# Performance work log

Hardware: AMD Instinct MI355X
Metric: run time of the kernel (lower is better)

The kernel has to match this reference:

```python
import jax, jax.numpy as jnp
import numpy as np

N, I, C, P, K = 16, 4096, 16, 16, 8
NI = N * I
E_RAND = 524288
CP = C + P


def setup_inputs() -> dict:
    key = jax.random.key(0)
    ks = jax.random.split(key, 14)
    x = jax.random.normal(ks[0], (N, I, C), dtype=jnp.float32)
    # random edges (stand-in for data-dependent kmeans complete subgraphs) + self loops
    src = jax.random.randint(ks[1], (E_RAND,), 0, NI)
    dst = jax.random.randint(ks[2], (E_RAND,), 0, NI)
    loops = jnp.arange(NI)
    edge_index = jnp.stack([jnp.concatenate([src, loops]),
                            jnp.concatenate([dst, loops])], axis=0)  # [2, E]
    # cluster labels: point p of cloud n -> cluster (p % K) + n*K, every cluster non-empty
    cluster_index = (jnp.arange(NI) % K) + (jnp.arange(NI) // I) * K
    sC = 1.0 / np.sqrt(C)
    sCP = 1.0 / np.sqrt(CP)
    return {
        "x": x,
        "edge_index": edge_index,
        "cluster_index": cluster_index,
        "F_W": jax.random.normal(ks[3], (C, C * CP), dtype=jnp.float32) * sC,
        "F_b": jnp.zeros((C * CP,), dtype=jnp.float32),
        "W_W": jax.random.normal(ks[4], (C, C * CP), dtype=jnp.float32) * sC,
        "W_b": jnp.zeros((C * CP,), dtype=jnp.float32),
        "M_W": jax.random.normal(ks[5], (CP, 1), dtype=jnp.float32) * sCP,
        "M_b": jnp.zeros((1,), dtype=jnp.float32),
        "B": jax.random.normal(ks[6], (CP,), dtype=jnp.float32),
        "mlp1_W": jax.random.normal(ks[7], (CP, CP), dtype=jnp.float32) * sCP,
        "mlp1_b": jnp.zeros((CP,), dtype=jnp.float32),
        "mlp2_W": jax.random.normal(ks[8], (CP, CP), dtype=jnp.float32) * sCP,
        "mlp2_b": jnp.zeros((CP,), dtype=jnp.float32),
        "sc_W": jax.random.normal(ks[9], (CP, CP), dtype=jnp.float32) * sCP,
        "sc_b": jnp.zeros((CP,), dtype=jnp.float32),
        "lr": jnp.asarray(1.0, dtype=jnp.float32),
    }


def _shrinking_unit(x, edge_index, cluster_index,
                    F_W, F_b, W_W, W_b, M_W, M_b, B,
                    mlp1_W, mlp1_b, mlp2_W, mlp2_b, sc_W, sc_b, lr):
    xf = x.reshape(-1, C)                      # [NI, C]
    src, dst = edge_index[0], edge_index[1]    # message flows src(j) -> dst(i)
    x_i = xf[dst]                              # [E, C]
    x_j = xf[src]
    # message: per-edge transform matrix F(x_j - x_i) in R^{(C+P) x C} applied to x_i
    msg = ((x_j - x_i) @ F_W + F_b).reshape(-1, CP, C)   # [E, CP, C]
    msg = jnp.einsum('epc,ec->ep', msg, x_i)             # [E, CP]
    # mean aggregation over incoming edges (self-loops guarantee deg >= 1)
    deg = jax.ops.segment_sum(jnp.ones_like(dst, dtype=x.dtype), dst, num_segments=NI)
    aggr = jax.ops.segment_sum(msg, dst, num_segments=NI) / deg[:, None]   # [NI, CP]
    # update
    weight = aggr @ M_W + M_b                             # [NI, 1]
    aggr = aggr * weight
    transform = (xf @ W_W + W_b).reshape(-1, CP, C)       # [NI, CP, C]
    aggr = aggr + jnp.einsum('npc,nc->np', transform, xf)
    conv = jax.nn.sigmoid(aggr + B).reshape(N, I, CP)     # [N, I, CP]
    # Aggregation module: pad x to CP, squeeze-excite style softmax gate
    x_pad = jnp.pad(x, ((0, 0), (0, 0), (0, P)))          # [N, I, CP]
    S1 = jnp.mean(x_pad, axis=1)                          # [N, CP]
    S2 = jnp.mean(conv, axis=1)
    Z1 = S1 @ mlp1_W + mlp1_b
    Z2 = S2 @ mlp2_W + mlp2_b
    M = jax.nn.softmax(jnp.stack([Z1, Z2], axis=0), axis=0)  # [2, N, CP]
    fused = M[0][:, None, :] * x_pad + M[1][:, None, :] * conv  # [N, I, CP]
    # MaxPool over clusters
    pooled = jax.ops.segment_max(fused.reshape(-1, CP), cluster_index,
                                 num_segments=K * N).reshape(N, K, CP)
    # SelfCorrelation: residual MLP scaled by learnable lambda
    pf = pooled.reshape(-1, CP)
    out = (pf + lr * (pf @ sc_W + sc_b)).reshape(N, K, CP)
    return out


def reference(x, edge_index, cluster_index, F_W, F_b, W_W, W_b, M_W, M_b, B,
              mlp1_W, mlp1_b, mlp2_W, mlp2_b, sc_W, sc_b, lr):
    return _shrinking_unit(x, edge_index, cluster_index, F_W, F_b, W_W, W_b,
                           M_W, M_b, B, mlp1_W, mlp1_b, mlp2_W, mlp2_b,
                           sc_W, sc_b, lr)
```

## Files before the change

### kernel.cpp

```cpp
#include <hip/hip_runtime.h>
#include <hip/hip_bf16.h>


#define POOL_NBLK 256

__device__ __forceinline__ unsigned fmap(float f) {
    unsigned u = __float_as_uint(f);
    return (u & 0x80000000u) ? ~u : (u | 0x80000000u);
}
__device__ __forceinline__ float funmap(unsigned m) {
    return (m & 0x80000000u) ? __uint_as_float(m & 0x7FFFFFFFu)
                             : __uint_as_float(~m);
}

__device__ __forceinline__ void load16(const float* __restrict__ p, float* r) {
    const float4* q = (const float4*)p;
    float4 a = q[0], b = q[1], c = q[2], d = q[3];
    r[0]=a.x; r[1]=a.y; r[2]=a.z; r[3]=a.w;
    r[4]=b.x; r[5]=b.y; r[6]=b.z; r[7]=b.w;
    r[8]=c.x; r[9]=c.y; r[10]=c.z; r[11]=c.w;
    r[12]=d.x; r[13]=d.y; r[14]=d.z; r[15]=d.w;
}

__global__ __launch_bounds__(256) void edge_scatter(
    const float* __restrict__ x, const int* __restrict__ ei,
    float* __restrict__ s, float* __restrict__ deg, int E)
{
    int tid = blockIdx.x * 256 + threadIdx.x;
    int e = tid >> 4, c = tid & 15;
    if (e >= E) return;
    int src = ei[e];
    int dst = ei[E + e];
    atomicAdd(&s[(size_t)dst * 16 + c], x[(size_t)src * 16 + c]);
    if (c == 0) atomicAdd(&deg[dst], 1.0f);
}

__global__ __launch_bounds__(128) void node_update(
    const float* __restrict__ x, const float* __restrict__ s,
    const float* __restrict__ deg,
    const float* __restrict__ Fw, const float* __restrict__ Fb,
    const float* __restrict__ Ww, const float* __restrict__ Wb,
    const float* __restrict__ Mw, const float* __restrict__ Mb,
    const float* __restrict__ Bv,
    float* __restrict__ conv, float* __restrict__ S1s, float* __restrict__ S2s)
{
    __shared__ float wlds[8192];
    __shared__ float aF[128 * 34];
    const int tid = threadIdx.x;

    {
        const float4* F4 = (const float4*)Fw;
        float4* w4 = (float4*)wlds;
        #pragma unroll
        for (int k = 0; k < 16; ++k) w4[k * 128 + tid] = F4[k * 128 + tid];
    }

    const int lane = tid & 63;
    const int h    = tid >> 6;
    const int i0   = blockIdx.x * 128 + lane;
    const int i1   = i0 + 64;
    const int n    = i0 >> 12;

    float xr0[16], tr0[16], xr1[16], tr1[16];
    load16(x + (size_t)i0 * 16, xr0);
    load16(s + (size_t)i0 * 16, tr0);
    load16(x + (size_t)i1 * 16, xr1);
    load16(s + (size_t)i1 * 16, tr1);
    const float invd0 = 1.0f / deg[i0];
    const float invd1 = 1.0f / deg[i1];
    #pragma unroll
    for (int c = 0; c < 16; ++c) {
        tr0[c] = tr0[c] * invd0 - xr0[c];
        tr1[c] = tr1[c] * invd1 - xr1[c];
    }

    __syncthreads();

    const int pbase = h << 8;
    #pragma unroll 1
    for (int pp = 0; pp < 16; ++pp) {
        const int cb0 = pbase + (pp << 4);
        float acc0 = 0.0f, acc1 = 0.0f;
        #pragma unroll
        for (int cb = 0; cb < 16; cb += 4) {
            const float b0 = Fb[cb0+cb+0], b1 = Fb[cb0+cb+1];
            const float b2 = Fb[cb0+cb+2], b3 = Fb[cb0+cb+3];
            float u00=b0,u01=b1,u02=b2,u03=b3;
            float u10=b0,u11=b1,u12=b2,u13=b3;
            #pragma unroll
            for (int cp = 0; cp < 16; ++cp) {
                const float4 f = *(const float4*)&wlds[(cp << 9) + cb0 + cb];
                u00 = fmaf(tr0[cp], f.x, u00);
                u01 = fmaf(tr0[cp], f.y, u01);
                u02 = fmaf(tr0[cp], f.z, u02);
                u03 = fmaf(tr0[cp], f.w, u03);
                u10 = fmaf(tr1[cp], f.x, u10);
                u11 = fmaf(tr1[cp], f.y, u11);
                u12 = fmaf(tr1[cp], f.z, u12);
                u13 = fmaf(tr1[cp], f.w, u13);
            }
            acc0 = fmaf(xr0[cb+0], u00, acc0);
            acc0 = fmaf(xr0[cb+1], u01, acc0);
            acc0 = fmaf(xr0[cb+2], u02, acc0);
            acc0 = fmaf(xr0[cb+3], u03, acc0);
            acc1 = fmaf(xr1[cb+0], u10, acc1);
            acc1 = fmaf(xr1[cb+1], u11, acc1);
            acc1 = fmaf(xr1[cb+2], u12, acc1);
            acc1 = fmaf(xr1[cb+3], u13, acc1);
        }
        aF[tid * 34 + pp]      = acc0;
        aF[tid * 34 + 17 + pp] = acc1;
    }
    __syncthreads();
    {
        const float4* W4 = (const float4*)Ww;
        float4* w4 = (float4*)wlds;
        #pragma unroll
        for (int k = 0; k < 16; ++k) w4[k * 128 + tid] = W4[k * 128 + tid];
    }

    float wgt0 = Mb[0], wgt1 = Mb[0];
    {
        const int r0 = lane * 34;
        const int r1 = (64 + lane) * 34;
        #pragma unroll
        for (int q = 0; q < 16; ++q) {
            wgt0 = fmaf(aF[r0 + q],      Mw[q],      wgt0);
            wgt0 = fmaf(aF[r1 + q],      Mw[16 + q], wgt0);
            wgt1 = fmaf(aF[r0 + 17 + q], Mw[q],      wgt1);
            wgt1 = fmaf(aF[r1 + 17 + q], Mw[16 + q], wgt1);
        }
    }
    __syncthreads();

    #pragma unroll 1
    for (int pp = 0; pp < 16; ++pp) {
        const int cb0 = pbase + (pp << 4);
        float acc0 = 0.0f, acc1 = 0.0f;
        #pragma unroll
        for (int cb = 0; cb < 16; cb += 4) {
            const float b0 = Wb[cb0+cb+0], b1 = Wb[cb0+cb+1];
            const float b2 = Wb[cb0+cb+2], b3 = Wb[cb0+cb+3];
            float u00=b0,u01=b1,u02=b2,u03=b3;
            float u10=b0,u11=b1,u12=b2,u13=b3;
            #pragma unroll
            for (int cp = 0; cp < 16; ++cp) {
                const float4 f = *(const float4*)&wlds[(cp << 9) + cb0 + cb];
                u00 = fmaf(xr0[cp], f.x, u00);
                u01 = fmaf(xr0[cp], f.y, u01);
                u02 = fmaf(xr0[cp], f.z, u02);
                u03 = fmaf(xr0[cp], f.w, u03);
                u10 = fmaf(xr1[cp], f.x, u10);
                u11 = fmaf(xr1[cp], f.y, u11);
                u12 = fmaf(xr1[cp], f.z, u12);
                u13 = fmaf(xr1[cp], f.w, u13);
            }
            acc0 = fmaf(xr0[cb+0], u00, acc0);
            acc0 = fmaf(xr0[cb+1], u01, acc0);
            acc0 = fmaf(xr0[cb+2], u02, acc0);
            acc0 = fmaf(xr0[cb+3], u03, acc0);
            acc1 = fmaf(xr1[cb+0], u10, acc1);
            acc1 = fmaf(xr1[cb+1], u11, acc1);
            acc1 = fmaf(xr1[cb+2], u12, acc1);
            acc1 = fmaf(xr1[cb+3], u13, acc1);
        }
        const float bv = Bv[(h << 4) + pp];
        const float z0 = aF[tid * 34 + pp]      * wgt0 + acc0 + bv;
        const float z1 = aF[tid * 34 + 17 + pp] * wgt1 + acc1 + bv;
        const float cv0 = 1.0f / (1.0f + expf(-z0));
        const float cv1 = 1.0f / (1.0f + expf(-z1));
        conv[(size_t)i0 * 32 + (h << 4) + pp] = cv0;
        conv[(size_t)i1 * 32 + (h << 4) + pp] = cv1;
        float v = cv0 + cv1;
        v += __shfl_xor(v, 1);
        v += __shfl_xor(v, 2);
        v += __shfl_xor(v, 4);
        v += __shfl_xor(v, 8);
        v += __shfl_xor(v, 16);
        v += __shfl_xor(v, 32);
        if (lane == 0) atomicAdd(&S2s[n * 32 + (h << 4) + pp], v);
    }
    if (h == 0) {
        #pragma unroll
        for (int c = 0; c < 16; ++c) {
            float v = xr0[c] + xr1[c];
            v += __shfl_xor(v, 1);
            v += __shfl_xor(v, 2);
            v += __shfl_xor(v, 4);
            v += __shfl_xor(v, 8);
            v += __shfl_xor(v, 16);
            v += __shfl_xor(v, 32);
            if (lane == 0) atomicAdd(&S1s[n * 32 + c], v);
        }
    }
}

__global__ void gate_kernel(const float* __restrict__ S1s, const float* __restrict__ S2s,
    const float* __restrict__ m1W, const float* __restrict__ m1b,
    const float* __restrict__ m2W, const float* __restrict__ m2b,
    float* __restrict__ M0, float* __restrict__ M1, float invI)
{
    int t = threadIdx.x;
    int n = t >> 5, p = t & 31;
    float z1 = m1b[p], z2 = m2b[p];
    #pragma unroll
    for (int q = 0; q < 32; ++q) {
        z1 = fmaf(S1s[n * 32 + q] * invI, m1W[q * 32 + p], z1);
        z2 = fmaf(S2s[n * 32 + q] * invI, m2W[q * 32 + p], z2);
    }
    float m = fmaxf(z1, z2);
    float e1 = expf(z1 - m), e2 = expf(z2 - m);
    float inv = 1.0f / (e1 + e2);
    M0[t] = e1 * inv;
    M1[t] = e2 * inv;
}

__global__ __launch_bounds__(256) void pool_kernel(
    const float* __restrict__ x, const float* __restrict__ conv,
    const int* __restrict__ cl, const float* __restrict__ M0,
    const float* __restrict__ M1, unsigned* __restrict__ blkT,
    int NI, int nSlots)
{
    __shared__ unsigned utab[4096];
    const int tid = threadIdx.x;
    for (int t = tid; t < nSlots; t += 256) utab[t] = 0u;
    __syncthreads();

    for (int i = blockIdx.x * 256 + tid; i < NI; i += POOL_NBLK * 256) {
        int n = i >> 12;
        int c = cl[i];
        const float* m0 = M0 + n * 32;
        const float* m1 = M1 + n * 32;
        float cr[32];
        {
            const float4* q = (const float4*)(conv + (size_t)i * 32);
            #pragma unroll
            for (int b = 0; b < 8; ++b) {
                float4 v = q[b];
                cr[b*4+0] = v.x; cr[b*4+1] = v.y; cr[b*4+2] = v.z; cr[b*4+3] = v.w;
            }
        }
        float xr[16];
        load16(x + (size_t)i * 16, xr);
        unsigned* up = utab + (c << 5);
        #pragma unroll
        for (int p = 0; p < 16; ++p) {
            float f = fmaf(m0[p], xr[p], m1[p] * cr[p]);
            atomicMax(&up[p], fmap(f));
        }
        #pragma unroll
        for (int p = 16; p < 32; ++p) {
            float f = m1[p] * cr[p];
            atomicMax(&up[p], fmap(f));
        }
    }
    __syncthreads();
    unsigned* dst = blkT + (size_t)blockIdx.x * nSlots;
    for (int t = tid; t < nSlots; t += 256) dst[t] = utab[t];
}

__global__ __launch_bounds__(256) void pool_reduce(
    const unsigned* __restrict__ blkT, unsigned* __restrict__ pooledM, int nSlots)
{
    int t = blockIdx.x * 256 + threadIdx.x;
    if (t >= nSlots) return;
    unsigned m = 0u;
    #pragma unroll 8
    for (int b = 0; b < POOL_NBLK; ++b)
        m = max(m, blkT[(size_t)b * nSlots + t]);
    pooledM[t] = m;
}

__global__ void final_kernel(const unsigned* __restrict__ pooledM,
    const float* __restrict__ scW, const float* __restrict__ scb,
    const float* __restrict__ lr, float* __restrict__ out, int total)
{
    int t = blockIdx.x * 256 + threadIdx.x;
    if (t >= total) return;
    int g = t >> 5, p = t & 31;
    float acc = scb[p];
    float self = 0.0f;
    #pragma unroll
    for (int q = 0; q < 32; ++q) {
        float v = funmap(pooledM[g * 32 + q]);
        if (q == p) self = v;
        acc = fmaf(v, scW[q * 32 + p], acc);
    }
    out[t] = self + lr[0] * acc;
}

extern "C" void kernel_launch(void* const* d_in, const int* in_sizes, int n_in,
                              void* d_out, int out_size, void* d_ws, size_t ws_size,
                              hipStream_t stream)
{
    const float* x   = (const float*)d_in[0];
    const int*   ei  = (const int*)d_in[1];
    const int*   clus= (const int*)d_in[2];
    const float* Fw  = (const float*)d_in[3];
    const float* Fb  = (const float*)d_in[4];
    const float* Ww  = (const float*)d_in[5];
    const float* Wb  = (const float*)d_in[6];
    const float* Mw  = (const float*)d_in[7];
    const float* Mb  = (const float*)d_in[8];
    const float* Bv  = (const float*)d_in[9];
    const float* m1W = (const float*)d_in[10];
    const float* m1b = (const float*)d_in[11];
    const float* m2W = (const float*)d_in[12];
    const float* m2b = (const float*)d_in[13];
    const float* scW = (const float*)d_in[14];
    const float* scb = (const float*)d_in[15];
    const float* lr  = (const float*)d_in[16];

    const int NI = in_sizes[0] / 16;
    const int E  = in_sizes[1] / 2;
    const int nG = NI >> 12;
    const int nC = out_size / 32;
    const int nSlots = nC * 32;

    float* ws   = (float*)d_ws;
    float* s_   = ws;
    float* deg_ = s_ + (size_t)NI * 16;
    float* S1s  = deg_ + NI;
    float* S2s  = S1s + nG * 32;
    unsigned* pooledM = (unsigned*)(S2s + nG * 32);
    float* M0   = (float*)(pooledM + nSlots);
    float* M1   = M0 + nG * 32;
    float* conv = M1 + nG * 32;
    unsigned* blkT = (unsigned*)s_;

    size_t need_bytes = (size_t)((char*)(conv + (size_t)NI * 32) - (char*)ws);
    if (ws_size < need_bytes || nSlots > 4096) return;
    if ((size_t)POOL_NBLK * nSlots > (size_t)NI * 16) return;

    size_t zbytes = (size_t)((char*)(pooledM + nSlots) - (char*)ws);
    hipMemsetAsync(d_ws, 0, zbytes, stream);

    edge_scatter<<<dim3((E * 16 + 255) / 256), dim3(256), 0, stream>>>(x, ei, s_, deg_, E);
    node_update<<<dim3(NI / 128), dim3(128), 0, stream>>>(
        x, s_, deg_, Fw, Fb, Ww, Wb, Mw, Mb, Bv, conv, S1s, S2s);
    gate_kernel<<<dim3(1), dim3(nG * 32), 0, stream>>>(
        S1s, S2s, m1W, m1b, m2W, m2b, M0, M1, 1.0f / 4096.0f);
    pool_kernel<<<dim3(POOL_NBLK), dim3(256), 0, stream>>>(
        x, conv, clus, M0, M1, blkT, NI, nSlots);
    pool_reduce<<<dim3((nSlots + 255) / 256), dim3(256), 0, stream>>>(
        blkT, pooledM, nSlots);
    final_kernel<<<dim3((out_size + 255) / 256), dim3(256), 0, stream>>>(
        pooledM, scW, scb, lr, (float*)d_out, out_size);
}
```

Measured before the change: 268.6 us.

## Split node_update output columns across four waves per 128-node block

node_update now runs 256 threads per block instead of 128, with each wave computing 8 output channels instead of 16 for the same 128 nodes. This halves the serial per-thread loop and doubles the waves available to hide LDS and memory latency. The cost is that every wave redundantly loads and normalizes the same node features, and the attention-weight reduction now reads partial sums from all four waves.

```diff
diff --git a/kernel.cpp b/kernel.cpp
--- a/kernel.cpp
+++ b/kernel.cpp
@@ -35,7 +35,7 @@
     if (c == 0) atomicAdd(&deg[dst], 1.0f);
 }
 
-__global__ __launch_bounds__(128) void node_update(
+__global__ __launch_bounds__(256) void node_update(
     const float* __restrict__ x, const float* __restrict__ s,
     const float* __restrict__ deg,
     const float* __restrict__ Fw, const float* __restrict__ Fb,
@@ -45,18 +45,19 @@
     float* __restrict__ conv, float* __restrict__ S1s, float* __restrict__ S2s)
 {
     __shared__ float wlds[8192];
-    __shared__ float aF[128 * 34];
+    __shared__ float aF[256 * 17];
     const int tid = threadIdx.x;
 
     {
         const float4* F4 = (const float4*)Fw;
         float4* w4 = (float4*)wlds;
         #pragma unroll
-        for (int k = 0; k < 16; ++k) w4[k * 128 + tid] = F4[k * 128 + tid];
+        for (int k = 0; k < 8; ++k) w4[k * 256 + tid] = F4[k * 256 + tid];
     }
 
     const int lane = tid & 63;
-    const int h    = tid >> 6;
+    const int ph   = (tid >> 6) & 1;
+    const int h    = tid >> 7;
     const int i0   = blockIdx.x * 128 + lane;
     const int i1   = i0 + 64;
     const int n    = i0 >> 12;
@@ -76,10 +77,10 @@
 
     __syncthreads();
 
-    const int pbase = h << 8;
+    const int colbase = (h << 8) + (ph << 7);
     #pragma unroll 1
-    for (int pp = 0; pp < 16; ++pp) {
-        const int cb0 = pbase + (pp << 4);
+    for (int pp = 0; pp < 8; ++pp) {
+        const int cb0 = colbase + (pp << 4);
         float acc0 = 0.0f, acc1 = 0.0f;
         #pragma unroll
         for (int cb = 0; cb < 16; cb += 4) {
@@ -108,34 +109,33 @@
             acc1 = fmaf(xr1[cb+2], u12, acc1);
             acc1 = fmaf(xr1[cb+3], u13, acc1);
         }
-        aF[tid * 34 + pp]      = acc0;
-        aF[tid * 34 + 17 + pp] = acc1;
+        aF[tid * 17 + pp]     = acc0;
+        aF[tid * 17 + 8 + pp] = acc1;
     }
     __syncthreads();
     {
         const float4* W4 = (const float4*)Ww;
         float4* w4 = (float4*)wlds;
         #pragma unroll
-        for (int k = 0; k < 16; ++k) w4[k * 128 + tid] = W4[k * 128 + tid];
+        for (int k = 0; k < 8; ++k) w4[k * 256 + tid] = W4[k * 256 + tid];
     }
 
     float wgt0 = Mb[0], wgt1 = Mb[0];
-    {
-        const int r0 = lane * 34;
-        const int r1 = (64 + lane) * 34;
-        #pragma unroll
-        for (int q = 0; q < 16; ++q) {
-            wgt0 = fmaf(aF[r0 + q],      Mw[q],      wgt0);
-            wgt0 = fmaf(aF[r1 + q],      Mw[16 + q], wgt0);
-            wgt1 = fmaf(aF[r0 + 17 + q], Mw[q],      wgt1);
-            wgt1 = fmaf(aF[r1 + 17 + q], Mw[16 + q], wgt1);
+    #pragma unroll
+    for (int wv = 0; wv < 4; ++wv) {
+        const int base = (wv * 64 + lane) * 17;
+        const int qoff = wv * 8;
+        #pragma unroll
+        for (int q = 0; q < 8; ++q) {
+            wgt0 = fmaf(aF[base + q],     Mw[qoff + q], wgt0);
+            wgt1 = fmaf(aF[base + 8 + q], Mw[qoff + q], wgt1);
         }
     }
     __syncthreads();
 
     #pragma unroll 1
-    for (int pp = 0; pp < 16; ++pp) {
-        const int cb0 = pbase + (pp << 4);
+    for (int pp = 0; pp < 8; ++pp) {
+        const int cb0 = colbase + (pp << 4);
         float acc0 = 0.0f, acc1 = 0.0f;
         #pragma unroll
         for (int cb = 0; cb < 16; cb += 4) {
@@ -164,13 +164,14 @@
             acc1 = fmaf(xr1[cb+2], u12, acc1);
             acc1 = fmaf(xr1[cb+3], u13, acc1);
         }
-        const float bv = Bv[(h << 4) + pp];
-        const float z0 = aF[tid * 34 + pp]      * wgt0 + acc0 + bv;
-        const float z1 = aF[tid * 34 + 17 + pp] * wgt1 + acc1 + bv;
+        const int pcol = (h << 4) + (ph << 3) + pp;
+        const float bv = Bv[pcol];
+        const float z0 = aF[tid * 17 + pp]     * wgt0 + acc0 + bv;
+        const float z1 = aF[tid * 17 + 8 + pp] * wgt1 + acc1 + bv;
         const float cv0 = 1.0f / (1.0f + expf(-z0));
         const float cv1 = 1.0f / (1.0f + expf(-z1));
-        conv[(size_t)i0 * 32 + (h << 4) + pp] = cv0;
-        conv[(size_t)i1 * 32 + (h << 4) + pp] = cv1;
+        conv[(size_t)i0 * 32 + pcol] = cv0;
+        conv[(size_t)i1 * 32 + pcol] = cv1;
         float v = cv0 + cv1;
         v += __shfl_xor(v, 1);
         v += __shfl_xor(v, 2);
@@ -178,9 +179,9 @@
         v += __shfl_xor(v, 8);
         v += __shfl_xor(v, 16);
         v += __shfl_xor(v, 32);
-        if (lane == 0) atomicAdd(&S2s[n * 32 + (h << 4) + pp], v);
-    }
-    if (h == 0) {
+        if (lane == 0) atomicAdd(&S2s[n * 32 + pcol], v);
+    }
+    if (tid < 64) {
         #pragma unroll
         for (int c = 0; c < 16; ++c) {
             float v = xr0[c] + xr1[c];
@@ -336,7 +337,7 @@
     hipMemsetAsync(d_ws, 0, zbytes, stream);
 
     edge_scatter<<<dim3((E * 16 + 255) / 256), dim3(256), 0, stream>>>(x, ei, s_, deg_, E);
-    node_update<<<dim3(NI / 128), dim3(128), 0, stream>>>(
+    node_update<<<dim3(NI / 128), dim3(256), 0, stream>>>(
         x, s_, deg_, Fw, Fb, Ww, Wb, Mw, Mb, Bv, conv, S1s, S2s);
     gate_kernel<<<dim3(1), dim3(nG * 32), 0, stream>>>(
         S1s, S2s, m1W, m1b, m2W, m2b, M0, M1, 1.0f / 4096.0f);
```

New measurement: 223.6 us. -16.8%, faster.
